# Kernel tuning notes

Hardware: AMD Instinct MI355X
Metric: run time of the kernel (lower is better)

The kernel has to match this reference:

```python
import jax, jax.numpy as jnp
import numpy as np
from jax import lax

B, T = 2048, 256
V, E, H = 128, 128, 64
POS_WEIGHT = 20.0


def setup_inputs() -> dict:
    key = jax.random.key(0)
    ks = jax.random.split(key, 9)
    # indices in [1, V) so padding_idx=0 row (zeroed) is unused
    x = jax.random.randint(ks[0], (B, T), 1, V)
    targets = (jax.random.uniform(ks[1], (B,)) < 0.05).astype(jnp.float32)
    emb = jax.random.normal(ks[2], (V, E), dtype=jnp.float32).at[0].set(0.0)  # padding_idx=0
    k = 1.0 / np.sqrt(H)
    W_ih = jax.random.uniform(ks[3], (4 * H, E), minval=-k, maxval=k, dtype=jnp.float32)
    W_hh = jax.random.uniform(ks[4], (4 * H, H), minval=-k, maxval=k, dtype=jnp.float32)
    b_ih = jax.random.uniform(ks[5], (4 * H,), minval=-k, maxval=k, dtype=jnp.float32)
    b_hh = jax.random.uniform(ks[6], (4 * H,), minval=-k, maxval=k, dtype=jnp.float32)
    W_fc = jax.random.uniform(ks[7], (1, H), minval=-k, maxval=k, dtype=jnp.float32)
    b_fc = jax.random.uniform(ks[8], (1,), minval=-k, maxval=k, dtype=jnp.float32)
    return {"x": x, "targets": targets, "emb": emb, "W_ih": W_ih, "W_hh": W_hh,
            "b_ih": b_ih, "b_hh": b_hh, "W_fc": W_fc, "b_fc": b_fc}


def reference(x, targets, emb, W_ih, W_hh, b_ih, b_hh, W_fc, b_fc):
    xe = emb[x]  # [B, T, E]
    # precompute input-to-hidden projections for all timesteps: [B, T, 4H]
    xp = jnp.einsum('bte,ge->btg', xe, W_ih) + b_ih + b_hh
    h0 = jnp.zeros((xe.shape[0], W_hh.shape[1]), dtype=xe.dtype)
    c0 = jnp.zeros_like(h0)

    def step(carry, xt):
        h, c = carry
        gates = xt + h @ W_hh.T  # [B, 4H], PyTorch gate order: i, f, g, o
        i, f, g, o = jnp.split(gates, 4, axis=-1)
        c = jax.nn.sigmoid(f) * c + jax.nn.sigmoid(i) * jnp.tanh(g)
        h = jax.nn.sigmoid(o) * jnp.tanh(c)
        return (h, c), None

    (hT, _), _ = lax.scan(step, (h0, c0), jnp.swapaxes(xp, 0, 1))  # scan over time
    logits = (hT @ W_fc.T + b_fc)[:, 0]  # [B]
    # BCEWithLogits with pos_weight, mean reduction (numerically stable)
    loss = -(POS_WEIGHT * targets * jax.nn.log_sigmoid(logits)
             + (1.0 - targets) * jax.nn.log_sigmoid(-logits)).mean()
    return logits, loss
```

## Files before the change

### kernel.cpp

```cpp
#include <hip/hip_runtime.h>
#include <stdint.h>

#define B_ 2048
#define T_ 256
#define V_ 128
#define E_ 128
#define H_ 64
#define G4_ 256
#define POS_W 20.0f
#define MB_ 4
#define NBLK_ (B_ / MB_)
typedef _Float16 half1;
typedef __attribute__((ext_vector_type(8))) _Float16 f16x8;
typedef __attribute__((ext_vector_type(4))) float f32x4;

#if __has_builtin(__builtin_amdgcn_exp2f)
#define EXP2F(x) __builtin_amdgcn_exp2f(x)
#else
#define EXP2F(x) exp2f(x)
#endif

#if __has_builtin(__builtin_amdgcn_rcpf)
#define RCPF(x) __builtin_amdgcn_rcpf(x)
#else
#define RCPF(x) (1.0f / (x))
#endif

#define L2E 1.44269504f

__device__ __forceinline__ void lds_barrier() {
    asm volatile("s_waitcnt lgkmcnt(0)\n\ts_barrier" ::: "memory");
}

__global__ void k_prep(const float* __restrict__ emb, const float* __restrict__ Wih,
                       const float* __restrict__ bih, const float* __restrict__ bhh,
                       float* __restrict__ projC, float* __restrict__ loss_slot) {
    int tid = threadIdx.x;
    int v = blockIdx.x;
    if (v == 0 && tid == 0) *loss_slot = 0.0f;
    int u = tid >> 2, g = tid & 3;
    int row = g * 64 + u;
    const float4* e4 = (const float4*)(emb + v * E_);
    const float4* w4 = (const float4*)(Wih + row * E_);
    float acc = bih[row] + bhh[row];
#pragma unroll
    for (int i = 0; i < E_ / 4; ++i) {
        float4 a = e4[i];
        float4 b = w4[i];
        acc += a.x * b.x + a.y * b.y + a.z * b.z + a.w * b.w;
    }
    projC[v * G4_ + tid] = acc;
}

__launch_bounds__(256, 2)
__global__ void k_lstm(const int* __restrict__ x, const float* __restrict__ Whh,
                       const float* __restrict__ projC, const float* __restrict__ Wfc,
                       const float* __restrict__ bfc, const float* __restrict__ targets,
                       float* __restrict__ logits, float* __restrict__ loss_slot) {
    int b0 = blockIdx.x * MB_;
    int t = threadIdx.x;
    int w = t >> 6, l = t & 63;
    int q = l >> 4, cc = l & 15;
    int u = 16 * w + cc;

    __shared__ __align__(16) half1 hf[2][1024];
    __shared__ int xT[T_][MB_];
    __shared__ float hfin[MB_][68];
    __shared__ float zred[MB_];

#pragma unroll
    for (int i = 0; i < MB_; ++i) xT[t][i] = x[(b0 + i) * T_ + t] << 10;
    ((float*)hf)[t] = 0.0f;
    ((float*)hf)[t + 256] = 0.0f;
    ((float*)hf)[t + 512] = 0.0f;
    ((float*)hf)[t + 768] = 0.0f;
    __syncthreads();

    f16x8 bf[4][2];
#pragma unroll
    for (int jj = 0; jj < 4; ++jj) {
#pragma unroll
        for (int c = 0; c < 2; ++c) {
            int row = jj * 64 + 16 * w + cc;
            int kb = c * 32 + q * 8;
            float4 w0 = *(const float4*)(Whh + row * H_ + kb);
            float4 w1 = *(const float4*)(Whh + row * H_ + kb + 4);
            f16x8 tmp;
            tmp[0] = (half1)w0.x; tmp[1] = (half1)w0.y;
            tmp[2] = (half1)w0.z; tmp[3] = (half1)w0.w;
            tmp[4] = (half1)w1.x; tmp[5] = (half1)w1.y;
            tmp[6] = (half1)w1.z; tmp[7] = (half1)w1.w;
            bf[jj][c] = tmp;
        }
    }

    int hbase = (u >> 5) * 512 + ((u >> 3) & 3) * 128 + (4 * q) * 8 + (u & 7);

    float cA = 0.0f, hA = 0.0f;
    const char* pcb = (const char*)projC;
    int uoff = u << 4;

    f32x4 ppA = *(const f32x4*)(pcb + xT[0][q] + uoff);
    f32x4 pnA = *(const f32x4*)(pcb + xT[1][q] + uoff);
    int xcA = xT[2][q];

    const f32x4 z4 = {0.0f, 0.0f, 0.0f, 0.0f};
    int p = 0;
#pragma unroll 2
    for (int step = 0; step < T_; ++step) {
        const f16x8 a0 = *(const f16x8*)(hf[p] + l * 8);
        const f16x8 a1 = *(const f16x8*)(hf[p] + 512 + l * 8);

        float gA[4];
#pragma unroll
        for (int jj = 0; jj < 4; ++jj) {
            f32x4 c4 = z4;
            c4[0] = ppA[jj];
            f32x4 d0 = __builtin_amdgcn_mfma_f32_16x16x32_f16(a0, bf[jj][0], c4, 0, 0, 0);
            f32x4 d1 = __builtin_amdgcn_mfma_f32_16x16x32_f16(a1, bf[jj][1], z4, 0, 0, 0);
            gA[jj] = d0[0] + d1[0];
        }

        f32x4 p2A = *(const f32x4*)(pcb + xcA + uoff);
        int xnA = xT[(step + 3) & (T_ - 1)][q];

        float ei = EXP2F(-L2E * gA[0]);
        float ef = EXP2F(-L2E * gA[1]);
        float eg = EXP2F(2.0f * L2E * gA[2]);
        float eo = EXP2F(-L2E * gA[3]);

        float onei = 1.0f + ei;
        float oneg = eg + 1.0f;
        float onef = 1.0f + ef;
        float P = onei * oneg;
        float D1 = P * onef;
        float N1 = __builtin_fmaf(cA, P, (eg - 1.0f) * onef);
        cA = N1 * RCPF(D1);

        float ct = fminf(fmaxf(cA, -15.0f), 15.0f);
        float et = EXP2F(2.0f * L2E * ct);
        float D2 = (1.0f + eo) * (et + 1.0f);
        hA = (et - 1.0f) * RCPF(D2);

        hf[p ^ 1][hbase] = (half1)hA;

        ppA = pnA;
        pnA = p2A;
        xcA = xnA;
        p ^= 1;
        lds_barrier();
    }

    hfin[q][u] = hA;
    __syncthreads();
    int m4 = t >> 6, uu = t & 63;
    float part = hfin[m4][uu] * Wfc[uu];
#pragma unroll
    for (int off = 32; off > 0; off >>= 1) part += __shfl_down(part, off, 64);
    if (uu == 0) {
        float z = part + bfc[0];
        logits[b0 + m4] = z;
        float tg = targets[b0 + m4];
        float e = EXP2F(-L2E * fabsf(z));
        float lsp = fminf(z, 0.0f) - log1pf(e);
        float lsn = lsp - z;
        zred[m4] = -(POS_W * tg * lsp + (1.0f - tg) * lsn) * (1.0f / (float)B_);
    }
    __syncthreads();
    if (t == 0) {
        float s = 0.0f;
#pragma unroll
        for (int i = 0; i < MB_; ++i) s += zred[i];
        atomicAdd(loss_slot, s);
    }
}

extern "C" void kernel_launch(void* const* d_in, const int* in_sizes, int n_in,
                              void* d_out, int out_size, void* d_ws, size_t ws_size,
                              hipStream_t stream) {
    const int* x = (const int*)d_in[0];
    const float* targets = (const float*)d_in[1];
    const float* emb = (const float*)d_in[2];
    const float* Wih = (const float*)d_in[3];
    const float* Whh = (const float*)d_in[4];
    const float* bih = (const float*)d_in[5];
    const float* bhh = (const float*)d_in[6];
    const float* Wfc = (const float*)d_in[7];
    const float* bfc = (const float*)d_in[8];
    float* out = (float*)d_out;

    float* projC = (float*)d_ws;

    k_prep<<<dim3(V_), dim3(256), 0, stream>>>(emb, Wih, bih, bhh, projC, out + B_);
    k_lstm<<<dim3(NBLK_), dim3(256), 0, stream>>>(x, Whh, projC, Wfc, bfc, targets, out,
                                                  out + B_);
}
```

Measured before the change: 155.1 us.

## Prescale gate weights by exp2 constants and add rotated-loop variant for half the blocks

Result: slower. 163.1 us (+5.2%).

```diff
diff --git a/kernel.cpp b/kernel.cpp
--- a/kernel.cpp
+++ b/kernel.cpp
@@ -32,6 +32,25 @@
     asm volatile("s_waitcnt lgkmcnt(0)\n\ts_barrier" ::: "memory");
 }
 
+__device__ __forceinline__ void cell_update(float g0, float g1, float g2, float g3,
+                                            float& cA, float& hA) {
+    float ei = EXP2F(g0);
+    float ef = EXP2F(g1);
+    float eg = EXP2F(g2);
+    float eo = EXP2F(g3);
+    float onei = 1.0f + ei;
+    float oneg = eg + 1.0f;
+    float onef = 1.0f + ef;
+    float P = onei * oneg;
+    float D1 = P * onef;
+    float N1 = __builtin_fmaf(cA, P, (eg - 1.0f) * onef);
+    cA = N1 * RCPF(D1);
+    float ct = fminf(fmaxf(cA, -15.0f), 15.0f);
+    float et = EXP2F(2.0f * L2E * ct);
+    float D2 = (1.0f + eo) * (et + 1.0f);
+    hA = (et - 1.0f) * RCPF(D2);
+}
+
 __global__ void k_prep(const float* __restrict__ emb, const float* __restrict__ Wih,
                        const float* __restrict__ bih, const float* __restrict__ bhh,
                        float* __restrict__ projC, float* __restrict__ loss_slot) {
@@ -49,7 +68,8 @@
         float4 b = w4[i];
         acc += a.x * b.x + a.y * b.y + a.z * b.z + a.w * b.w;
     }
-    projC[v * G4_ + tid] = acc;
+    float s = (g == 2) ? (2.0f * L2E) : (-L2E);
+    projC[v * G4_ + tid] = acc * s;
 }
 
 __launch_bounds__(256, 2)
@@ -79,6 +99,7 @@
     f16x8 bf[4][2];
 #pragma unroll
     for (int jj = 0; jj < 4; ++jj) {
+        float s = (jj == 2) ? (2.0f * L2E) : (-L2E);
 #pragma unroll
         for (int c = 0; c < 2; ++c) {
             int row = jj * 64 + 16 * w + cc;
@@ -86,10 +107,10 @@
             float4 w0 = *(const float4*)(Whh + row * H_ + kb);
             float4 w1 = *(const float4*)(Whh + row * H_ + kb + 4);
             f16x8 tmp;
-            tmp[0] = (half1)w0.x; tmp[1] = (half1)w0.y;
-            tmp[2] = (half1)w0.z; tmp[3] = (half1)w0.w;
-            tmp[4] = (half1)w1.x; tmp[5] = (half1)w1.y;
-            tmp[6] = (half1)w1.z; tmp[7] = (half1)w1.w;
+            tmp[0] = (half1)(w0.x * s); tmp[1] = (half1)(w0.y * s);
+            tmp[2] = (half1)(w0.z * s); tmp[3] = (half1)(w0.w * s);
+            tmp[4] = (half1)(w1.x * s); tmp[5] = (half1)(w1.y * s);
+            tmp[6] = (half1)(w1.z * s); tmp[7] = (half1)(w1.w * s);
             bf[jj][c] = tmp;
         }
     }
@@ -105,50 +126,76 @@
     int xcA = xT[2][q];
 
     const f32x4 z4 = {0.0f, 0.0f, 0.0f, 0.0f};
-    int p = 0;
+    int role = (blockIdx.x >> 8) & 1;
+
+    if (role == 0) {
+        int p = 0;
 #pragma unroll 2
-    for (int step = 0; step < T_; ++step) {
-        const f16x8 a0 = *(const f16x8*)(hf[p] + l * 8);
-        const f16x8 a1 = *(const f16x8*)(hf[p] + 512 + l * 8);
-
-        float gA[4];
-#pragma unroll
-        for (int jj = 0; jj < 4; ++jj) {
-            f32x4 c4 = z4;
-            c4[0] = ppA[jj];
-            f32x4 d0 = __builtin_amdgcn_mfma_f32_16x16x32_f16(a0, bf[jj][0], c4, 0, 0, 0);
-            f32x4 d1 = __builtin_amdgcn_mfma_f32_16x16x32_f16(a1, bf[jj][1], z4, 0, 0, 0);
-            gA[jj] = d0[0] + d1[0];
-        }
-
-        f32x4 p2A = *(const f32x4*)(pcb + xcA + uoff);
-        int xnA = xT[(step + 3) & (T_ - 1)][q];
-
-        float ei = EXP2F(-L2E * gA[0]);
-        float ef = EXP2F(-L2E * gA[1]);
-        float eg = EXP2F(2.0f * L2E * gA[2]);
-        float eo = EXP2F(-L2E * gA[3]);
-
-        float onei = 1.0f + ei;
-        float oneg = eg + 1.0f;
-        float onef = 1.0f + ef;
-        float P = onei * oneg;
-        float D1 = P * onef;
-        float N1 = __builtin_fmaf(cA, P, (eg - 1.0f) * onef);
-        cA = N1 * RCPF(D1);
-
-        float ct = fminf(fmaxf(cA, -15.0f), 15.0f);
-        float et = EXP2F(2.0f * L2E * ct);
-        float D2 = (1.0f + eo) * (et + 1.0f);
-        hA = (et - 1.0f) * RCPF(D2);
-
-        hf[p ^ 1][hbase] = (half1)hA;
-
-        ppA = pnA;
-        pnA = p2A;
-        xcA = xnA;
-        p ^= 1;
-        lds_barrier();
+        for (int step = 0; step < T_; ++step) {
+            const f16x8 a0 = *(const f16x8*)(hf[p] + l * 8);
+            const f16x8 a1 = *(const f16x8*)(hf[p] + 512 + l * 8);
+            float gA[4];
+#pragma unroll
+            for (int jj = 0; jj < 4; ++jj) {
+                f32x4 c4 = z4;
+                c4[0] = ppA[jj];
+                f32x4 d0 = __builtin_amdgcn_mfma_f32_16x16x32_f16(a0, bf[jj][0], c4, 0, 0, 0);
+                f32x4 d1 = __builtin_amdgcn_mfma_f32_16x16x32_f16(a1, bf[jj][1], z4, 0, 0, 0);
+                gA[jj] = d0[0] + d1[0];
+            }
+            f32x4 p2A = *(const f32x4*)(pcb + xcA + uoff);
+            int xnA = xT[(step + 3) & (T_ - 1)][q];
+            cell_update(gA[0], gA[1], gA[2], gA[3], cA, hA);
+            hf[p ^ 1][hbase] = (half1)hA;
+            ppA = pnA; pnA = p2A; xcA = xnA;
+            p ^= 1;
+            lds_barrier();
+        }
+    } else {
+        f32x4 d0[4], d1[4];
+        {
+            const f16x8 a0 = *(const f16x8*)(hf[0] + l * 8);
+            const f16x8 a1 = *(const f16x8*)(hf[0] + 512 + l * 8);
+#pragma unroll
+            for (int jj = 0; jj < 4; ++jj) {
+                f32x4 c4 = z4;
+                c4[0] = ppA[jj];
+                d0[jj] = __builtin_amdgcn_mfma_f32_16x16x32_f16(a0, bf[jj][0], c4, 0, 0, 0);
+                d1[jj] = __builtin_amdgcn_mfma_f32_16x16x32_f16(a1, bf[jj][1], z4, 0, 0, 0);
+            }
+            f32x4 p2A = *(const f32x4*)(pcb + xcA + uoff);
+            int xnA = xT[3][q];
+            ppA = pnA; pnA = p2A; xcA = xnA;
+        }
+#pragma unroll 2
+        for (int step = 1; step < T_; ++step) {
+            float g0 = d0[0][0] + d1[0][0];
+            float g1 = d0[1][0] + d1[1][0];
+            float g2 = d0[2][0] + d1[2][0];
+            float g3 = d0[3][0] + d1[3][0];
+            cell_update(g0, g1, g2, g3, cA, hA);
+            hf[step & 1][hbase] = (half1)hA;
+            lds_barrier();
+            const f16x8 a0 = *(const f16x8*)(hf[step & 1] + l * 8);
+            const f16x8 a1 = *(const f16x8*)(hf[step & 1] + 512 + l * 8);
+#pragma unroll
+            for (int jj = 0; jj < 4; ++jj) {
+                f32x4 c4 = z4;
+                c4[0] = ppA[jj];
+                d0[jj] = __builtin_amdgcn_mfma_f32_16x16x32_f16(a0, bf[jj][0], c4, 0, 0, 0);
+                d1[jj] = __builtin_amdgcn_mfma_f32_16x16x32_f16(a1, bf[jj][1], z4, 0, 0, 0);
+            }
+            f32x4 p2A = *(const f32x4*)(pcb + xcA + uoff);
+            int xnA = xT[(step + 3) & (T_ - 1)][q];
+            ppA = pnA; pnA = p2A; xcA = xnA;
+        }
+        {
+            float g0 = d0[0][0] + d1[0][0];
+            float g1 = d0[1][0] + d1[1][0];
+            float g2 = d0[2][0] + d1[2][0];
+            float g3 = d0[3][0] + d1[3][0];
+            cell_update(g0, g1, g2, g3, cA, hA);
+        }
     }
 
     hfin[q][u] = hA;
```

## Pack 16 sequences per block to fill MFMA rows, prescale gate weights

Applied to the files above, without the earlier changes.

Measured after the change: 214.3 us. +38.2%, slower.

```diff
diff --git a/kernel.cpp b/kernel.cpp
--- a/kernel.cpp
+++ b/kernel.cpp
@@ -8,7 +8,7 @@
 #define H_ 64
 #define G4_ 256
 #define POS_W 20.0f
-#define MB_ 4
+#define MB_ 16
 #define NBLK_ (B_ / MB_)
 typedef _Float16 half1;
 typedef __attribute__((ext_vector_type(8))) _Float16 f16x8;
@@ -30,6 +30,25 @@
 
 __device__ __forceinline__ void lds_barrier() {
     asm volatile("s_waitcnt lgkmcnt(0)\n\ts_barrier" ::: "memory");
+}
+
+__device__ __forceinline__ void cell_update(float g0, float g1, float g2, float g3,
+                                            float& cA, float& hA) {
+    float ei = EXP2F(g0);
+    float ef = EXP2F(g1);
+    float eg = EXP2F(g2);
+    float eo = EXP2F(g3);
+    float onei = 1.0f + ei;
+    float oneg = eg + 1.0f;
+    float onef = 1.0f + ef;
+    float P = onei * oneg;
+    float D1 = P * onef;
+    float N1 = __builtin_fmaf(cA, P, (eg - 1.0f) * onef);
+    cA = N1 * RCPF(D1);
+    float ct = fminf(fmaxf(cA, -15.0f), 15.0f);
+    float et = EXP2F(2.0f * L2E * ct);
+    float D2 = (1.0f + eo) * (et + 1.0f);
+    hA = (et - 1.0f) * RCPF(D2);
 }
 
 __global__ void k_prep(const float* __restrict__ emb, const float* __restrict__ Wih,
@@ -49,10 +68,11 @@
         float4 b = w4[i];
         acc += a.x * b.x + a.y * b.y + a.z * b.z + a.w * b.w;
     }
-    projC[v * G4_ + tid] = acc;
-}
-
-__launch_bounds__(256, 2)
+    float s = (g == 2) ? (2.0f * L2E) : (-L2E);
+    projC[v * G4_ + tid] = acc * s;
+}
+
+__launch_bounds__(256, 1)
 __global__ void k_lstm(const int* __restrict__ x, const float* __restrict__ Whh,
                        const float* __restrict__ projC, const float* __restrict__ Wfc,
                        const float* __restrict__ bfc, const float* __restrict__ targets,
@@ -79,6 +99,7 @@
     f16x8 bf[4][2];
 #pragma unroll
     for (int jj = 0; jj < 4; ++jj) {
+        float s = (jj == 2) ? (2.0f * L2E) : (-L2E);
 #pragma unroll
         for (int c = 0; c < 2; ++c) {
             int row = jj * 64 + 16 * w + cc;
@@ -86,23 +107,29 @@
             float4 w0 = *(const float4*)(Whh + row * H_ + kb);
             float4 w1 = *(const float4*)(Whh + row * H_ + kb + 4);
             f16x8 tmp;
-            tmp[0] = (half1)w0.x; tmp[1] = (half1)w0.y;
-            tmp[2] = (half1)w0.z; tmp[3] = (half1)w0.w;
-            tmp[4] = (half1)w1.x; tmp[5] = (half1)w1.y;
-            tmp[6] = (half1)w1.z; tmp[7] = (half1)w1.w;
+            tmp[0] = (half1)(w0.x * s); tmp[1] = (half1)(w0.y * s);
+            tmp[2] = (half1)(w0.z * s); tmp[3] = (half1)(w0.w * s);
+            tmp[4] = (half1)(w1.x * s); tmp[5] = (half1)(w1.y * s);
+            tmp[6] = (half1)(w1.z * s); tmp[7] = (half1)(w1.w * s);
             bf[jj][c] = tmp;
         }
     }
 
     int hbase = (u >> 5) * 512 + ((u >> 3) & 3) * 128 + (4 * q) * 8 + (u & 7);
 
-    float cA = 0.0f, hA = 0.0f;
+    float creg[4] = {0.f, 0.f, 0.f, 0.f};
+    float hreg[4] = {0.f, 0.f, 0.f, 0.f};
     const char* pcb = (const char*)projC;
     int uoff = u << 4;
 
-    f32x4 ppA = *(const f32x4*)(pcb + xT[0][q] + uoff);
-    f32x4 pnA = *(const f32x4*)(pcb + xT[1][q] + uoff);
-    int xcA = xT[2][q];
+    f32x4 pp[4], pn[4];
+    int xc[4];
+#pragma unroll
+    for (int r = 0; r < 4; ++r) {
+        pp[r] = *(const f32x4*)(pcb + xT[0][4 * q + r] + uoff);
+        pn[r] = *(const f32x4*)(pcb + xT[1][4 * q + r] + uoff);
+        xc[r] = xT[2][4 * q + r];
+    }
 
     const f32x4 z4 = {0.0f, 0.0f, 0.0f, 0.0f};
     int p = 0;
@@ -111,60 +138,59 @@
         const f16x8 a0 = *(const f16x8*)(hf[p] + l * 8);
         const f16x8 a1 = *(const f16x8*)(hf[p] + 512 + l * 8);
 
-        float gA[4];
+        f32x4 d[4];
 #pragma unroll
         for (int jj = 0; jj < 4; ++jj) {
-            f32x4 c4 = z4;
-            c4[0] = ppA[jj];
-            f32x4 d0 = __builtin_amdgcn_mfma_f32_16x16x32_f16(a0, bf[jj][0], c4, 0, 0, 0);
-            f32x4 d1 = __builtin_amdgcn_mfma_f32_16x16x32_f16(a1, bf[jj][1], z4, 0, 0, 0);
-            gA[jj] = d0[0] + d1[0];
-        }
-
-        f32x4 p2A = *(const f32x4*)(pcb + xcA + uoff);
-        int xnA = xT[(step + 3) & (T_ - 1)][q];
-
-        float ei = EXP2F(-L2E * gA[0]);
-        float ef = EXP2F(-L2E * gA[1]);
-        float eg = EXP2F(2.0f * L2E * gA[2]);
-        float eo = EXP2F(-L2E * gA[3]);
-
-        float onei = 1.0f + ei;
-        float oneg = eg + 1.0f;
-        float onef = 1.0f + ef;
-        float P = onei * oneg;
-        float D1 = P * onef;
-        float N1 = __builtin_fmaf(cA, P, (eg - 1.0f) * onef);
-        cA = N1 * RCPF(D1);
-
-        float ct = fminf(fmaxf(cA, -15.0f), 15.0f);
-        float et = EXP2F(2.0f * L2E * ct);
-        float D2 = (1.0f + eo) * (et + 1.0f);
-        hA = (et - 1.0f) * RCPF(D2);
-
-        hf[p ^ 1][hbase] = (half1)hA;
-
-        ppA = pnA;
-        pnA = p2A;
-        xcA = xnA;
+            f32x4 d0 = __builtin_amdgcn_mfma_f32_16x16x32_f16(a0, bf[jj][0], z4, 0, 0, 0);
+            d[jj] = __builtin_amdgcn_mfma_f32_16x16x32_f16(a1, bf[jj][1], d0, 0, 0, 0);
+        }
+
+        f32x4 p2[4];
+        int xn[4];
+#pragma unroll
+        for (int r = 0; r < 4; ++r) {
+            p2[r] = *(const f32x4*)(pcb + xc[r] + uoff);
+            xn[r] = xT[(step + 3) & (T_ - 1)][4 * q + r];
+        }
+
+#pragma unroll
+        for (int r = 0; r < 4; ++r) {
+            float g0 = d[0][r] + pp[r][0];
+            float g1 = d[1][r] + pp[r][1];
+            float g2 = d[2][r] + pp[r][2];
+            float g3 = d[3][r] + pp[r][3];
+            cell_update(g0, g1, g2, g3, creg[r], hreg[r]);
+            hf[p ^ 1][hbase + 8 * r] = (half1)hreg[r];
+        }
+
+#pragma unroll
+        for (int r = 0; r < 4; ++r) {
+            pp[r] = pn[r];
+            pn[r] = p2[r];
+            xc[r] = xn[r];
+        }
         p ^= 1;
         lds_barrier();
     }
 
-    hfin[q][u] = hA;
+#pragma unroll
+    for (int r = 0; r < 4; ++r) hfin[4 * q + r][u] = hreg[r];
     __syncthreads();
-    int m4 = t >> 6, uu = t & 63;
-    float part = hfin[m4][uu] * Wfc[uu];
-#pragma unroll
-    for (int off = 32; off > 0; off >>= 1) part += __shfl_down(part, off, 64);
-    if (uu == 0) {
-        float z = part + bfc[0];
-        logits[b0 + m4] = z;
-        float tg = targets[b0 + m4];
-        float e = EXP2F(-L2E * fabsf(z));
-        float lsp = fminf(z, 0.0f) - log1pf(e);
-        float lsn = lsp - z;
-        zred[m4] = -(POS_W * tg * lsp + (1.0f - tg) * lsn) * (1.0f / (float)B_);
+#pragma unroll
+    for (int rr = 0; rr < 4; ++rr) {
+        int row = 4 * w + rr;
+        float part = hfin[row][l] * Wfc[l];
+#pragma unroll
+        for (int off = 32; off > 0; off >>= 1) part += __shfl_down(part, off, 64);
+        if (l == 0) {
+            float z = part + bfc[0];
+            logits[b0 + row] = z;
+            float tg = targets[b0 + row];
+            float e = EXP2F(-L2E * fabsf(z));
+            float lsp = fminf(z, 0.0f) - log1pf(e);
+            float lsn = lsp - z;
+            zred[row] = -(POS_W * tg * lsp + (1.0f - tg) * lsn) * (1.0f / (float)B_);
+        }
     }
     __syncthreads();
     if (t == 0) {
```
